# Kernel tuning notes

Measured on AMD Instinct MI355X. Metric: run time of the kernel, lower is better.

Reference implementation:

```python
import math
import jax, jax.numpy as jnp
import numpy as np

N_EMBD = 1024
N_HEAD = 16
NUM_BUCKETS = 32
MAX_DISTANCE = 128


def _relative_position_bucket(relative_position, num_buckets=NUM_BUCKETS, max_distance=MAX_DISTANCE):
    # unidirectional (bidirectional=False): rp = -min(rp, 0)
    rp = -jnp.minimum(relative_position, 0)
    max_exact = num_buckets // 2
    is_small = rp < max_exact
    rp_large = max_exact + (
        jnp.log(rp.astype(jnp.float32) / max_exact + 1e-10)
        / math.log(max_distance / max_exact)
        * (num_buckets - max_exact)
    ).astype(jnp.int32)
    rp_large = jnp.minimum(rp_large, num_buckets - 1)
    return jnp.where(is_small, rp, rp_large)


def setup_inputs() -> dict:
    key = jax.random.key(0)
    ks = jax.random.split(key, 6)
    B, T, C = 4, 2048, N_EMBD
    s_in = 1.0 / math.sqrt(C)
    x = jax.random.normal(ks[0], (B, T, C), dtype=jnp.float32)
    W_attn = jax.random.normal(ks[1], (3 * C, C), dtype=jnp.float32) * s_in
    b_attn = jnp.zeros((3 * C,), dtype=jnp.float32)
    W_proj = jax.random.normal(ks[2], (C, C), dtype=jnp.float32) * s_in
    b_proj = jnp.zeros((C,), dtype=jnp.float32)
    rel_emb = jax.random.normal(ks[3], (NUM_BUCKETS, N_HEAD), dtype=jnp.float32) * 0.02
    return {"x": x, "W_attn": W_attn, "b_attn": b_attn,
            "W_proj": W_proj, "b_proj": b_proj, "rel_emb": rel_emb}


def reference(x, W_attn, b_attn, W_proj, b_proj, rel_emb):
    B, T, C = x.shape
    H = N_HEAD
    D = C // H
    qkv = x @ W_attn.T + b_attn              # [B,T,3C]
    q, k, v = jnp.split(qkv, 3, axis=-1)
    q = q.reshape(B, T, H, D).transpose(0, 2, 1, 3)  # [B,H,T,D]
    k = k.reshape(B, T, H, D).transpose(0, 2, 1, 3)
    v = v.reshape(B, T, H, D).transpose(0, 2, 1, 3)

    # T5 relative position bias (unidirectional)
    pos = jnp.arange(T)
    rel_pos = pos[None, :] - pos[:, None]            # [T,T] key - query
    buckets = _relative_position_bucket(rel_pos)     # [T,T]
    rel_bias = rel_emb[buckets]                      # [T,T,H]
    rel_bias = rel_bias.transpose(2, 0, 1)[None]     # [1,H,T,T]

    att = jnp.einsum('bhqd,bhkd->bhqk', q, k) * (1.0 / math.sqrt(D))
    att = att + rel_bias
    causal = jnp.tril(jnp.ones((T, T), dtype=bool))
    att = jnp.where(causal[None, None], att, -jnp.inf)
    att = jax.nn.softmax(att, axis=-1)
    y = jnp.einsum('bhqk,bhkd->bhqd', att, v)        # [B,H,T,D]
    y = y.transpose(0, 2, 1, 3).reshape(B, T, C)
    y = y @ W_proj.T + b_proj
    return y
```

## Files before the change

### kernel.cpp

```cpp
#include <hip/hip_runtime.h>
#include <hip/hip_bf16.h>

typedef __attribute__((ext_vector_type(8))) short short8;
typedef __attribute__((ext_vector_type(4))) short short4v;
typedef __attribute__((ext_vector_type(4))) float f32x4;

#define DEVI static __device__ __forceinline__

#define MTOK 8192
#define CDIM 1024
#define HN 16
#define HD 64
#define TSEQ 2048

#if defined(__has_builtin)
#if __has_builtin(__builtin_amdgcn_exp2f)
#define EXP2(x) __builtin_amdgcn_exp2f(x)
#else
#define EXP2(x) exp2f(x)
#endif
#else
#define EXP2(x) exp2f(x)
#endif

DEVI short bf16_rne(float f) {
  union { float f; unsigned u; } v; v.f = f;
  unsigned r = v.u + 0x7FFFu + ((v.u >> 16) & 1u);
  return (short)(r >> 16);
}

DEVI unsigned cvt_pk_bf16(float lo, float hi) {
  unsigned r;
  asm("v_cvt_pk_bf16_f32 %0, %1, %2" : "=v"(r) : "v"(lo), "v"(hi));
  return r;
}

DEVI void gload16(const void* g, void* l) {
  __builtin_amdgcn_global_load_lds(
      (const __attribute__((address_space(1))) void*)(unsigned long long)g,
      (__attribute__((address_space(3))) void*)(unsigned long long)l, 16, 0, 0);
}

#define MFMA_B16(A,B,C) __builtin_amdgcn_mfma_f32_16x16x32_bf16(A,B,C,0,0,0)

__global__ void pack_kernel(const float* __restrict__ x, const float* __restrict__ Wa,
                            const float* __restrict__ Wp,
                            short* __restrict__ xb, short* __restrict__ wab,
                            short* __restrict__ wpb) {
  const int NX4 = MTOK*CDIM/4, NA4 = 3*CDIM*CDIM/4, NP4 = CDIM*CDIM/4;
  const int total = NX4 + NA4 + NP4;
  for (int i = blockIdx.x*blockDim.x + threadIdx.x; i < total; i += gridDim.x*blockDim.x) {
    const float* src; short* dst; int off;
    if (i < NX4)          { src = x;  dst = xb;  off = i*4; }
    else if (i < NX4+NA4) { src = Wa; dst = wab; off = (i-NX4)*4; }
    else                  { src = Wp; dst = wpb; off = (i-NX4-NA4)*4; }
    float4 v = *(const float4*)(src + off);
    short4v r;
    r.x = bf16_rne(v.x); r.y = bf16_rne(v.y); r.z = bf16_rne(v.z); r.w = bf16_rne(v.w);
    *(short4v*)(dst + off) = r;
  }
}

__global__ void bias_table_kernel(const float* __restrict__ rel_emb, float* __restrict__ tab) {
  int d = blockIdx.x*blockDim.x + threadIdx.x;
  if (d >= TSEQ) return;
  int bucket;
  if (d < 16) bucket = d;
  else {
    int bl = 16 + (int)(logf((float)d / 16.0f + 1e-10f) / 2.0794415416798357f * 16.0f);
    bucket = bl < 31 ? bl : 31;
  }
  for (int h = 0; h < HN; h++) tab[h*TSEQ + d] = rel_emb[bucket*HN + h];
}

template<int EPI>
__global__ __launch_bounds__(256)
void gemm_bt(const short* __restrict__ A, const short* __restrict__ B,
             const float* __restrict__ bias,
             short* __restrict__ oq, short* __restrict__ ok, short* __restrict__ ov,
             float* __restrict__ of) {
  const int K = CDIM;
  int nbx = gridDim.x;
  int idx = blockIdx.y * nbx + blockIdx.x;
  int cpx = (nbx * gridDim.y) >> 3;
  int sw = (idx & 7) * cpx + (idx >> 3);
  int n0 = (sw % nbx) * 128, m0 = (sw / nbx) * 128;

  int tid = threadIdx.x;
  int lane = tid & 63, w = tid >> 6;
  int wr = w >> 1, wc = w & 1;
  int r16 = lane & 15, g = lane >> 4;

  __shared__ __align__(16) short As[128*32];
  __shared__ __align__(16) short Bs[128*32];

  f32x4 zf = {0.f, 0.f, 0.f, 0.f};
  f32x4 acc[4][4];
  #pragma unroll
  for (int m = 0; m < 4; m++)
    #pragma unroll
    for (int n = 0; n < 4; n++) acc[m][n] = zf;

  int sr = tid >> 2;
  int sc = (tid & 3) * 8;
  const short* ga = A + (long long)(m0 + sr) * K + sc;
  const short* gb = B + (long long)(n0 + sr) * K + sc;
  short* la = As + sr*32 + sc;
  short* lb = Bs + sr*32 + sc;

  for (int k0 = 0; k0 < K; k0 += 32) {
    gload16(ga + k0,           la);
    gload16(ga + k0 + 64*K,    la + 64*32);
    gload16(gb + k0,           lb);
    gload16(gb + k0 + 64*K,    lb + 64*32);
    __syncthreads();
    short8 af[4], bfv[4];
    #pragma unroll
    for (int m = 0; m < 4; m++)
      af[m] = *(const short8*)&As[(wr*64 + m*16 + r16)*32 + g*8];
    #pragma unroll
    for (int n = 0; n < 4; n++)
      bfv[n] = *(const short8*)&Bs[(wc*64 + n*16 + r16)*32 + g*8];
    #pragma unroll
    for (int m = 0; m < 4; m++)
      #pragma unroll
      for (int n = 0; n < 4; n++)
        acc[m][n] = MFMA_B16(af[m], bfv[n], acc[m][n]);
    __syncthreads();
  }

  #pragma unroll
  for (int mi = 0; mi < 4; mi++) {
    #pragma unroll
    for (int n = 0; n < 4; n++) {
      int col = n0 + wc*64 + n*16 + r16;
      float bv = bias[col];
      if constexpr (EPI == 0) {
        int which = col >> 10;
        int c = col & (CDIM-1);
        int hh = c >> 6, dd = c & 63;
        short* outp = (which == 0) ? oq : (which == 1) ? ok : ov;
        #pragma unroll
        for (int j = 0; j < 4; j++) {
          int row = m0 + wr*64 + mi*16 + g*4 + j;
          int b = row >> 11, t = row & (TSEQ-1);
          outp[(((long long)(b*HN + hh))*TSEQ + t)*HD + dd] = bf16_rne(acc[mi][n][j] + bv);
        }
      } else {
        #pragma unroll
        for (int j = 0; j < 4; j++) {
          int row = m0 + wr*64 + mi*16 + g*4 + j;
          of[(long long)row*CDIM + col] = acc[mi][n][j] + bv;
        }
      }
    }
  }
}

__global__ __launch_bounds__(256)
void vtrans_kernel(const short* __restrict__ vin, short* __restrict__ vout) {
  int bh = blockIdx.x >> 5;
  int t0 = (blockIdx.x & 31) * 64;
  __shared__ short tile[64][66];
  int tid = threadIdx.x;
  const short* src = vin + ((long long)bh*TSEQ + t0)*HD;
  #pragma unroll
  for (int i = 0; i < 2; i++) {
    int idx = tid + i*256;
    int r = idx >> 3, c = (idx & 7)*8;
    short8 v = *(const short8*)(src + r*HD + c);
    #pragma unroll
    for (int j = 0; j < 8; j++) tile[r][c+j] = v[j];
  }
  __syncthreads();
  short* dst = vout + (long long)bh*HD*TSEQ + t0;
  #pragma unroll
  for (int i = 0; i < 2; i++) {
    int idx = tid + i*256;
    int d = idx >> 3, c = (idx & 7)*8;
    short8 v;
    #pragma unroll
    for (int j = 0; j < 8; j++) v[j] = tile[c+j][d];
    *(short8*)(dst + (long long)d*TSEQ + c) = v;
  }
}

__global__ __launch_bounds__(256)
void attn_kernel(const short* __restrict__ Qg, const short* __restrict__ Kg,
                 const short* __restrict__ Vtg, const float* __restrict__ btab,
                 short* __restrict__ outp) {
  int bh = blockIdx.x;
  int qb = 15 - (int)blockIdx.y;
  int h = bh & (HN-1), b = bh >> 4;
  int q0 = qb * 128;
  int tid = threadIdx.x, lane = tid & 63, w = tid >> 6;
  int r16 = lane & 15, g = lane >> 4;

  __shared__ __align__(16) short Ks[64*64];
  __shared__ __align__(16) short Vs[64*64];
  __shared__ __align__(16) short Ps[8][1024];
  __shared__ float bias_s[256];

  bias_s[tid & 255] = btab[h*TSEQ + (tid & 255)] * 1.44269504f;
  float cb = btab[h*TSEQ + 255] * 1.44269504f;

  short8 qa[2][2];
  #pragma unroll
  for (int mi = 0; mi < 2; mi++)
    #pragma unroll
    for (int ks = 0; ks < 2; ks++)
      qa[mi][ks] = *(const short8*)(Qg + ((long long)bh*TSEQ + q0 + w*32 + mi*16 + r16)*HD + ks*32 + g*8);

  f32x4 zf = {0.f,0.f,0.f,0.f};
  f32x4 o[2][4];
  #pragma unroll
  for (int mi = 0; mi < 2; mi++)
    #pragma unroll
    for (int c = 0; c < 4; c++) o[mi][c] = zf;
  float m_[2] = {-1e30f, -1e30f}, l_[2] = {0.f, 0.f};

  const short8 ones = {0x3f80,0x3f80,0x3f80,0x3f80,0x3f80,0x3f80,0x3f80,0x3f80};
  int qmax_wave = q0 + w*32 + 31;
  int swz = r16 & 7;
  int qrel = q0 + w*32 + r16;
  const float SC = 0.18033688f;

  for (int kb = 0; kb < q0 + 128; kb += 64) {
    #pragma unroll
    for (int i = 0; i < 2; i++) {
      int idx = tid + i*256;
      int r = idx >> 3;
      int cq = ((idx & 7) ^ (r & 7)) * 8;
      gload16(Kg  + ((long long)bh*TSEQ + kb + r)*HD + cq, (short*)Ks + idx*8);
      gload16(Vtg + ((long long)bh*HD  + r)*TSEQ + kb + cq, (short*)Vs + idx*8);
    }
    __syncthreads();
    if (kb <= qmax_wave) {
      f32x4 s[2][4];
      #pragma unroll
      for (int mi = 0; mi < 2; mi++)
        #pragma unroll
        for (int n = 0; n < 4; n++) s[mi][n] = zf;
      #pragma unroll
      for (int n = 0; n < 4; n++) {
        #pragma unroll
        for (int ks = 0; ks < 2; ks++) {
          short8 kf = *(const short8*)&Ks[(n*16 + r16)*64 + ((ks*4 + g) ^ swz)*8];
          s[0][n] = MFMA_B16(kf, qa[0][ks], s[0][n]);
          s[1][n] = MFMA_B16(kf, qa[1][ks], s[1][n]);
        }
      }
      bool far = (kb + 176 <= q0 + w*32);
      #pragma unroll
      for (int mi = 0; mi < 2; mi++) {
        char* prow = (char*)Ps[w*2 + mi] + r16*128 + ((g & 1) << 3);
        if (far) {
          float smax = s[mi][0][0];
          #pragma unroll
          for (int n = 0; n < 4; n++)
            #pragma unroll
            for (int j = 0; j < 4; j++) smax = fmaxf(smax, s[mi][n][j]);
          float mx = smax*SC + cb;
          mx = fmaxf(mx, __shfl_xor(mx, 16));
          mx = fmaxf(mx, __shfl_xor(mx, 32));
          float mnew;
          if (__all(mx <= m_[mi] + 8.0f)) {
            mnew = m_[mi];
          } else {
            mnew = fmaxf(m_[mi], mx);
            float corr = EXP2(m_[mi] - mnew);
            l_[mi] *= corr;
            #pragma unroll
            for (int c = 0; c < 4; c++) o[mi][c] *= corr;
            m_[mi] = mnew;
          }
          float cc = cb - mnew;
          #pragma unroll
          for (int n = 0; n < 4; n++) {
            unsigned u0 = cvt_pk_bf16(EXP2(__builtin_fmaf(s[mi][n][0], SC, cc)),
                                      EXP2(__builtin_fmaf(s[mi][n][1], SC, cc)));
            unsigned u1 = cvt_pk_bf16(EXP2(__builtin_fmaf(s[mi][n][2], SC, cc)),
                                      EXP2(__builtin_fmaf(s[mi][n][3], SC, cc)));
            *(uint2*)(prow + ((((n*2 + (g >> 1)) ^ swz)) << 4)) = make_uint2(u0, u1);
          }
        } else {
          int dbase = qrel + mi*16 - kb - g*4;
          float rowv[4][4];
          #pragma unroll
          for (int n = 0; n < 4; n++)
            #pragma unroll
            for (int j = 0; j < 4; j++) {
              int d = dbase - n*16 - j;
              rowv[n][j] = (d >= 0) ? s[mi][n][j]*SC + bias_s[d] : -1e30f;
            }
          float mx = rowv[0][0];
          #pragma unroll
          for (int n = 0; n < 4; n++)
            #pragma unroll
            for (int j = 0; j < 4; j++) mx = fmaxf(mx, rowv[n][j]);
          mx = fmaxf(mx, __shfl_xor(mx, 16));
          mx = fmaxf(mx, __shfl_xor(mx, 32));
          float mnew;
          if (__all(mx <= m_[mi] + 8.0f)) {
            mnew = m_[mi];
          } else {
            mnew = fmaxf(m_[mi], mx);
            float corr = EXP2(m_[mi] - mnew);
            l_[mi] *= corr;
            #pragma unroll
            for (int c = 0; c < 4; c++) o[mi][c] *= corr;
            m_[mi] = mnew;
          }
          #pragma unroll
          for (int n = 0; n < 4; n++) {
            unsigned u0 = cvt_pk_bf16(EXP2(rowv[n][0] - mnew), EXP2(rowv[n][1] - mnew));
            unsigned u1 = cvt_pk_bf16(EXP2(rowv[n][2] - mnew), EXP2(rowv[n][3] - mnew));
            *(uint2*)(prow + ((((n*2 + (g >> 1)) ^ swz)) << 4)) = make_uint2(u0, u1);
          }
        }
      }
      f32x4 lacc[2] = {zf, zf};
      #pragma unroll
      for (int ks = 0; ks < 2; ks++) {
        short8 pf0 = *(const short8*)((char*)Ps[w*2+0] + r16*128 + (((ks*4 + g) ^ swz) << 4));
        short8 pf1 = *(const short8*)((char*)Ps[w*2+1] + r16*128 + (((ks*4 + g) ^ swz) << 4));
        lacc[0] = MFMA_B16(ones, pf0, lacc[0]);
        lacc[1] = MFMA_B16(ones, pf1, lacc[1]);
        #pragma unroll
        for (int c = 0; c < 4; c++) {
          short8 vf = *(const short8*)&Vs[(c*16 + r16)*64 + ((ks*4 + g) ^ swz)*8];
          o[0][c] = MFMA_B16(vf, pf0, o[0][c]);
          o[1][c] = MFMA_B16(vf, pf1, o[1][c]);
        }
      }
      l_[0] += lacc[0][0];
      l_[1] += lacc[1][0];
    }
    __syncthreads();
  }

  #pragma unroll
  for (int mi = 0; mi < 2; mi++) {
    float inv = 1.0f / l_[mi];
    long long base = ((long long)(b*TSEQ + qrel + mi*16))*CDIM + h*HD;
    #pragma unroll
    for (int c = 0; c < 4; c++) {
      #pragma unroll
      for (int jj = 0; jj < 2; jj++) {
        unsigned pv = cvt_pk_bf16(o[mi][c][jj*2]*inv, o[mi][c][jj*2+1]*inv);
        *(unsigned*)(outp + base + c*16 + g*4 + jj*2) = pv;
      }
    }
  }
}

extern "C" void kernel_launch(void* const* d_in, const int* in_sizes, int n_in,
                              void* d_out, int out_size, void* d_ws, size_t ws_size,
                              hipStream_t stream) {
  (void)in_sizes; (void)n_in; (void)out_size; (void)ws_size;
  const float* x      = (const float*)d_in[0];
  const float* W_attn = (const float*)d_in[1];
  const float* b_attn = (const float*)d_in[2];
  const float* W_proj = (const float*)d_in[3];
  const float* b_proj = (const float*)d_in[4];
  const float* rel    = (const float*)d_in[5];
  float* out = (float*)d_out;
  char* ws = (char*)d_ws;

  short* xb   = (short*)(ws);
  short* wab  = (short*)(ws + 16777216LL);
  short* wpb  = (short*)(ws + 23068672LL);
  short* qbuf = (short*)(ws + 25165824LL);
  short* kbuf = (short*)(ws + 41943040LL);
  short* vbuf = (short*)(ws + 58720256LL);
  short* att  = (short*)(ws + 75497472LL);
  float* tab  = (float*)(ws + 92274688LL);
  short* vt   = xb;

  pack_kernel<<<2048, 256, 0, stream>>>(x, W_attn, W_proj, xb, wab, wpb);
  bias_table_kernel<<<8, 256, 0, stream>>>(rel, tab);
  gemm_bt<0><<<dim3(24, 64), 256, 0, stream>>>(xb, wab, b_attn, qbuf, kbuf, vbuf, nullptr);
  vtrans_kernel<<<2048, 256, 0, stream>>>(vbuf, vt);
  attn_kernel<<<dim3(64, 16), 256, 0, stream>>>(qbuf, kbuf, vt, tab, att);
  gemm_bt<1><<<dim3(8, 64), 256, 0, stream>>>(att, wpb, b_proj, nullptr, nullptr, nullptr, out);
}
```

Measured before the change: 273.8 us.

## Pipeline GEMM with triple-buffered LDS, larger tiles, and fused V transpose

New measurement: 249.7 us. -8.8%, faster.

```diff
diff --git a/kernel.cpp b/kernel.cpp
--- a/kernel.cpp
+++ b/kernel.cpp
@@ -74,114 +74,114 @@
 }
 
 template<int EPI>
-__global__ __launch_bounds__(256)
-void gemm_bt(const short* __restrict__ A, const short* __restrict__ B,
-             const float* __restrict__ bias,
-             short* __restrict__ oq, short* __restrict__ ok, short* __restrict__ ov,
-             float* __restrict__ of) {
+__global__ __launch_bounds__(512)
+void gemm2(const short* __restrict__ A, const short* __restrict__ B,
+           const float* __restrict__ bias,
+           short* __restrict__ oq, short* __restrict__ ok, short* __restrict__ vt,
+           float* __restrict__ of) {
   const int K = CDIM;
   int nbx = gridDim.x;
   int idx = blockIdx.y * nbx + blockIdx.x;
   int cpx = (nbx * gridDim.y) >> 3;
   int sw = (idx & 7) * cpx + (idx >> 3);
-  int n0 = (sw % nbx) * 128, m0 = (sw / nbx) * 128;
-
-  int tid = threadIdx.x;
-  int lane = tid & 63, w = tid >> 6;
-  int wr = w >> 1, wc = w & 1;
+  int n0 = (sw % nbx) * 128, m0 = (sw / nbx) * 256;
+
+  int tid = threadIdx.x, lane = tid & 63, w = tid >> 6;
+  int wm = w >> 1, wn = w & 1;
   int r16 = lane & 15, g = lane >> 4;
 
-  __shared__ __align__(16) short As[128*32];
-  __shared__ __align__(16) short Bs[128*32];
-
-  f32x4 zf = {0.f, 0.f, 0.f, 0.f};
+  __shared__ __align__(16) short As[3][256*32];
+  __shared__ __align__(16) short Bs[3][128*32];
+
+  f32x4 zf = {0.f,0.f,0.f,0.f};
   f32x4 acc[4][4];
   #pragma unroll
-  for (int m = 0; m < 4; m++)
-    #pragma unroll
-    for (int n = 0; n < 4; n++) acc[m][n] = zf;
-
-  int sr = tid >> 2;
-  int sc = (tid & 3) * 8;
-  const short* ga = A + (long long)(m0 + sr) * K + sc;
-  const short* gb = B + (long long)(n0 + sr) * K + sc;
-  short* la = As + sr*32 + sc;
-  short* lb = Bs + sr*32 + sc;
-
-  for (int k0 = 0; k0 < K; k0 += 32) {
-    gload16(ga + k0,           la);
-    gload16(ga + k0 + 64*K,    la + 64*32);
-    gload16(gb + k0,           lb);
-    gload16(gb + k0 + 64*K,    lb + 64*32);
-    __syncthreads();
-    short8 af[4], bfv[4];
-    #pragma unroll
-    for (int m = 0; m < 4; m++)
-      af[m] = *(const short8*)&As[(wr*64 + m*16 + r16)*32 + g*8];
-    #pragma unroll
-    for (int n = 0; n < 4; n++)
-      bfv[n] = *(const short8*)&Bs[(wc*64 + n*16 + r16)*32 + g*8];
-    #pragma unroll
-    for (int m = 0; m < 4; m++)
-      #pragma unroll
-      for (int n = 0; n < 4; n++)
-        acc[m][n] = MFMA_B16(af[m], bfv[n], acc[m][n]);
-    __syncthreads();
-  }
-
-  #pragma unroll
-  for (int mi = 0; mi < 4; mi++) {
-    #pragma unroll
-    for (int n = 0; n < 4; n++) {
-      int col = n0 + wc*64 + n*16 + r16;
-      float bv = bias[col];
-      if constexpr (EPI == 0) {
-        int which = col >> 10;
-        int c = col & (CDIM-1);
-        int hh = c >> 6, dd = c & 63;
-        short* outp = (which == 0) ? oq : (which == 1) ? ok : ov;
-        #pragma unroll
-        for (int j = 0; j < 4; j++) {
-          int row = m0 + wr*64 + mi*16 + g*4 + j;
-          int b = row >> 11, t = row & (TSEQ-1);
-          outp[(((long long)(b*HN + hh))*TSEQ + t)*HD + dd] = bf16_rne(acc[mi][n][j] + bv);
+  for (int mf = 0; mf < 4; mf++)
+    #pragma unroll
+    for (int nf = 0; nf < 4; nf++) acc[mf][nf] = zf;
+
+  int r0 = tid >> 2;
+  int cswz = (((tid & 3) ^ ((r0 >> 1) & 3)) << 3);
+  long long aofs = (long long)(m0 + r0) * K + cswz;
+  long long bofs = (long long)(n0 + r0) * K + cswz;
+
+  auto STAGE = [&](int kt, int bi) {
+    gload16(A + aofs + kt*32,          (short*)As[bi] + tid*8);
+    gload16(A + aofs + kt*32 + 128*K,  (short*)As[bi] + 4096 + tid*8);
+    gload16(B + bofs + kt*32,          (short*)Bs[bi] + tid*8);
+  };
+
+  STAGE(0, 0); STAGE(1, 1);
+  asm volatile("s_waitcnt vmcnt(3)" ::: "memory");
+  __builtin_amdgcn_s_barrier();
+  __builtin_amdgcn_sched_barrier(0);
+
+  int swz3 = (r16 >> 1) & 3;
+  int fbA = (wm*64 + r16)*32 + ((g ^ swz3) << 3);
+  int fbB = (wn*64 + r16)*32 + ((g ^ swz3) << 3);
+
+  for (int kt = 0; kt < 32; kt++) {
+    int cur = kt % 3;
+    if (kt < 30) STAGE(kt + 2, (kt + 2) % 3);
+    const short* Ab = As[cur];
+    const short* Bb = Bs[cur];
+    short8 af[4], bf[4];
+    #pragma unroll
+    for (int mf = 0; mf < 4; mf++) af[mf] = *(const short8*)(Ab + fbA + mf*512);
+    #pragma unroll
+    for (int nf = 0; nf < 4; nf++) bf[nf] = *(const short8*)(Bb + fbB + nf*512);
+    __builtin_amdgcn_s_setprio(1);
+    #pragma unroll
+    for (int mf = 0; mf < 4; mf++)
+      #pragma unroll
+      for (int nf = 0; nf < 4; nf++)
+        acc[mf][nf] = MFMA_B16(af[mf], bf[nf], acc[mf][nf]);
+    __builtin_amdgcn_s_setprio(0);
+    if (kt < 30) asm volatile("s_waitcnt vmcnt(3)" ::: "memory");
+    else         asm volatile("s_waitcnt vmcnt(0)" ::: "memory");
+    __builtin_amdgcn_s_barrier();
+    __builtin_amdgcn_sched_barrier(0);
+  }
+
+  int b = m0 >> 11;
+  int mrel = (m0 & 2047) + wm*64 + g*4;
+  if constexpr (EPI == 0) {
+    int which = n0 >> 10;
+    int hh = ((n0 & 1023) >> 6) + wn;
+    long long bh = (long long)(b*HN + hh);
+    #pragma unroll
+    for (int nf = 0; nf < 4; nf++) {
+      int dd = nf*16 + r16;
+      float bv = bias[n0 + wn*64 + dd];
+      if (which == 2) {
+        short* vdst = vt + (bh*HD + dd)*TSEQ + mrel;
+        #pragma unroll
+        for (int mf = 0; mf < 4; mf++) {
+          short4v pv;
+          #pragma unroll
+          for (int j = 0; j < 4; j++) pv[j] = bf16_rne(acc[mf][nf][j] + bv);
+          *(short4v*)(vdst + mf*16) = pv;
         }
       } else {
-        #pragma unroll
-        for (int j = 0; j < 4; j++) {
-          int row = m0 + wr*64 + mi*16 + g*4 + j;
-          of[(long long)row*CDIM + col] = acc[mi][n][j] + bv;
-        }
-      }
-    }
-  }
-}
-
-__global__ __launch_bounds__(256)
-void vtrans_kernel(const short* __restrict__ vin, short* __restrict__ vout) {
-  int bh = blockIdx.x >> 5;
-  int t0 = (blockIdx.x & 31) * 64;
-  __shared__ short tile[64][66];
-  int tid = threadIdx.x;
-  const short* src = vin + ((long long)bh*TSEQ + t0)*HD;
-  #pragma unroll
-  for (int i = 0; i < 2; i++) {
-    int idx = tid + i*256;
-    int r = idx >> 3, c = (idx & 7)*8;
-    short8 v = *(const short8*)(src + r*HD + c);
-    #pragma unroll
-    for (int j = 0; j < 8; j++) tile[r][c+j] = v[j];
-  }
-  __syncthreads();
-  short* dst = vout + (long long)bh*HD*TSEQ + t0;
-  #pragma unroll
-  for (int i = 0; i < 2; i++) {
-    int idx = tid + i*256;
-    int d = idx >> 3, c = (idx & 7)*8;
-    short8 v;
-    #pragma unroll
-    for (int j = 0; j < 8; j++) v[j] = tile[c+j][d];
-    *(short8*)(dst + (long long)d*TSEQ + c) = v;
+        short* odst = (which == 0 ? oq : ok) + bh*TSEQ*HD + dd;
+        #pragma unroll
+        for (int mf = 0; mf < 4; mf++)
+          #pragma unroll
+          for (int j = 0; j < 4; j++)
+            odst[(long long)(mrel + mf*16 + j)*HD] = bf16_rne(acc[mf][nf][j] + bv);
+      }
+    }
+  } else {
+    #pragma unroll
+    for (int nf = 0; nf < 4; nf++) {
+      int col = n0 + wn*64 + nf*16 + r16;
+      float bv = bias[col];
+      #pragma unroll
+      for (int mf = 0; mf < 4; mf++)
+        #pragma unroll
+        for (int j = 0; j < 4; j++)
+          of[(long long)(m0 + wm*64 + mf*16 + g*4 + j)*CDIM + col] = acc[mf][nf][j] + bv;
+    }
   }
 }
 
@@ -372,15 +372,13 @@
   short* wpb  = (short*)(ws + 23068672LL);
   short* qbuf = (short*)(ws + 25165824LL);
   short* kbuf = (short*)(ws + 41943040LL);
-  short* vbuf = (short*)(ws + 58720256LL);
+  short* vt   = (short*)(ws + 58720256LL);
   short* att  = (short*)(ws + 75497472LL);
   float* tab  = (float*)(ws + 92274688LL);
-  short* vt   = xb;
 
   pack_kernel<<<2048, 256, 0, stream>>>(x, W_attn, W_proj, xb, wab, wpb);
   bias_table_kernel<<<8, 256, 0, stream>>>(rel, tab);
-  gemm_bt<0><<<dim3(24, 64), 256, 0, stream>>>(xb, wab, b_attn, qbuf, kbuf, vbuf, nullptr);
-  vtrans_kernel<<<2048, 256, 0, stream>>>(vbuf, vt);
+  gemm2<0><<<dim3(24, 32), 512, 0, stream>>>(xb, wab, b_attn, qbuf, kbuf, vt, nullptr);
   attn_kernel<<<dim3(64, 16), 256, 0, stream>>>(qbuf, kbuf, vt, tab, att);
-  gemm_bt<1><<<dim3(8, 64), 256, 0, stream>>>(att, wpb, b_proj, nullptr, nullptr, nullptr, out);
-}
+  gemm2<1><<<dim3(8, 32), 512, 0, stream>>>(att, wpb, b_proj, nullptr, nullptr, nullptr, out);
+}
```
